# Optimization experiments

Measured on AMD Instinct MI355X. Metric: run time of the kernel, lower is better.

Reference implementation:

```python
import jax, jax.numpy as jnp
import numpy as np

B, CIN, H, W = 32, 16, 64, 64
COUT, K, STRIDE = 32, 3, 1


def setup_inputs() -> dict:
    key = jax.random.key(0)
    k1, k2, k3 = jax.random.split(key, 3)
    x = jax.random.normal(k1, (B, CIN, H, W), dtype=jnp.float32)
    # per-location kernels (Ho, Wo, Cout, Cin, K, K); kaiming-ish scale
    fan_in = CIN * K * K
    bound = float(np.sqrt(3.0 / fan_in))
    weights = jax.random.uniform(k2, (H, W, COUT, CIN, K, K), dtype=jnp.float32,
                                 minval=-bound, maxval=bound)
    bias = jax.random.normal(k3, (H, W, COUT), dtype=jnp.float32)
    return {"x": x, "weights": weights, "bias": bias}


def reference(x, weights, bias):
    Ho, Wo, co, ci, k, _ = weights.shape
    pad = k // 2
    if k % 2 == 1:
        padding = [(pad, pad), (pad, pad)]
    else:
        padding = [(pad - 1, pad), (pad - 1, pad)]
    # im2col: (B, ci*k*k, Ho, Wo); feature dim ordered channel-slowest, matching
    # torch's (C, k, k) flatten after unfold+permute.
    patches = jax.lax.conv_general_dilated_patches(
        x, (k, k), (STRIDE, STRIDE), padding)
    w = weights.reshape(Ho, Wo, co, ci * k * k)
    # per-location matmul: out[b,o,h,w] = sum_p patches[b,p,h,w] * w[h,w,o,p]
    out = jnp.einsum('bphw,hwop->bohw', patches, w)
    out = out + bias.transpose(2, 0, 1)[None]  # (1, Cout, Ho, Wo)
    return out
```

## Files before the change

### kernel.cpp

```cpp
#include <hip/hip_runtime.h>


#define CIN     16
#define HH      64
#define WW      64
#define COUT    32
#define PP      144
#define WT      8
#define RSTRIDE 770

typedef float v4f  __attribute__((ext_vector_type(4)));
typedef float v16f __attribute__((ext_vector_type(16)));
typedef short v8s  __attribute__((ext_vector_type(8)));

__device__ __forceinline__ unsigned short f2bf(float f) {
    unsigned int u = __builtin_bit_cast(unsigned int, f);
    u += 0x7fffu + ((u >> 16) & 1u);
    return (unsigned short)(u >> 16);
}
__device__ __forceinline__ unsigned int pk2(float a, float b) {
    return (unsigned int)f2bf(a) | ((unsigned int)f2bf(b) << 16);
}

__global__ __launch_bounds__(512, 4) void xonv_kernel(
    const float* __restrict__ x,
    const float* __restrict__ weights,
    const float* __restrict__ bias,
    float* __restrict__ out)
{
    const int t  = threadIdx.x;
    const int bi = blockIdx.x;

    const int xcd  = bi & 7;
    const int rest = bi >> 3;
    const int wg   = rest & 7;
    const int h    = (rest >> 3) * 8 + xcd;
    const int w0   = wg * WT;
    const int wstart = w0 - 4;

    __shared__ alignas(16) unsigned char smraw[49280];
    unsigned short* xl = (unsigned short*)smraw;
    float*          ol = (float*)smraw;

    {
        const int rid0 = t >> 2;
        const int sub  = t & 3;
        int b  = rid0 / 48;
        int cr = rid0 % 48;
        const int col4  = wstart + sub * 4;
        const bool colok = (col4 >= 0) && (col4 <= WW - 4);
#pragma unroll
        for (int pass = 0; pass < 12; ++pass) {
            const int c   = cr / 3;
            const int r   = cr - c * 3;
            const int row = h + r - 1;
            float4 f = {0.f, 0.f, 0.f, 0.f};
            if (colok && (unsigned)row < HH) {
                f = *(const float4*)(x + ((size_t)(b * CIN + c)) * (HH * WW)
                                       + row * WW + col4);
            }
            unsigned int* d = (unsigned int*)(xl + b * RSTRIDE + cr * 16 + sub * 4);
            d[0] = pk2(f.x, f.y);
            d[1] = pk2(f.z, f.w);
            b += 2; cr += 32; if (cr >= 48) { cr -= 48; ++b; }
        }
    }
    __syncthreads();

    const int l  = t & 63;
    const int wv = t >> 6;
    const int w  = w0 + wv;
    const int o  = l & 31;
    const int kh = l >> 5;
    const int ph = kh * 8;

    const float* wp = weights + (size_t)(h * WW + w) * (COUT * PP)
                              + (size_t)o * PP + ph;
    const int xbase = (l & 31) * RSTRIDE + wv + 3;

    v16f acc;
#pragma unroll
    for (int i = 0; i < 16; ++i) acc[i] = 0.f;

    int dq = ph >> 2;
    int mq = ph >> 2;

    v4f c0 = *(const v4f*)(wp);
    v4f c1 = *(const v4f*)(wp + 4);

#pragma unroll
    for (int kc = 0; kc < 9; ++kc) {
        v4f n0, n1;
        if (kc < 8) {
            n0 = *(const v4f*)(wp + (kc + 1) * 16);
            n1 = *(const v4f*)(wp + (kc + 1) * 16 + 4);
        }

        v8s a;
        const int base = xbase + dq * 16 + mq;
#pragma unroll
        for (int j = 0; j < 8; ++j) {
            const int e  = mq + j;
            const int tt = (e * 11) >> 5;
            a[j] = (short)xl[base + j + 13 * tt];
        }

        union { unsigned int u[4]; v8s s; } ub;
        ub.u[0] = pk2(c0.x, c0.y); ub.u[1] = pk2(c0.z, c0.w);
        ub.u[2] = pk2(c1.x, c1.y); ub.u[3] = pk2(c1.z, c1.w);

        acc = __builtin_amdgcn_mfma_f32_32x32x16_bf16(a, ub.s, acc, 0, 0, 0);

        c0 = n0; c1 = n1;
        mq += 1; dq += 5; if (mq == 3) { mq = 0; dq += 1; }
    }

    const float bia = bias[(size_t)(h * WW + w) * COUT + o];

    __syncthreads();

#pragma unroll
    for (int r = 0; r < 16; ++r) {
        const int brow = (r & 3) + 8 * (r >> 2) + 4 * kh;
        ol[(brow * COUT + o) * 9 + wv] = acc[r] + bia;
    }
    __syncthreads();

    {
        const int seg = t >> 3;
        const int wj  = t & 7;
        float* ob = out + (size_t)h * WW + w0 + wj;
#pragma unroll
        for (int i = 0; i < 16; ++i) {
            const int bo = i * 64 + seg;
            ob[(size_t)bo * (HH * WW)] = ol[bo * 9 + wj];
        }
    }
}

extern "C" void kernel_launch(void* const* d_in, const int* in_sizes, int n_in,
                              void* d_out, int out_size, void* d_ws, size_t ws_size,
                              hipStream_t stream) {
    const float* x       = (const float*)d_in[0];
    const float* weights = (const float*)d_in[1];
    const float* bias    = (const float*)d_in[2];
    float* out           = (float*)d_out;
    (void)in_sizes; (void)n_in; (void)out_size; (void)d_ws; (void)ws_size;

    dim3 grid(512);
    dim3 block(512);
    hipLaunchKernelGGL(xonv_kernel, grid, block, 0, stream, x, weights, bias, out);
}
```

Baseline: 129.2 us.

## Widen blocks to 16 output columns with compile-time im2col offsets and float4 stores

Each block now covers 16 output columns per row with 1024 threads, which halves the grid and lowers the redundant halo loads of x per output. The shared-memory im2col layout is rebuilt so that gather offsets are compile-time constants, replacing the runtime index arithmetic. Weight prefetch goes two steps ahead, and the first weight loads are issued before the x staging so they overlap it. The epilogue is split into two halves that write float4 vectors to global memory, at the cost of extra barriers and a larger block that may reduce occupancy.

```diff
diff --git a/kernel.cpp b/kernel.cpp
--- a/kernel.cpp
+++ b/kernel.cpp
@@ -1,13 +1,11 @@
 #include <hip/hip_runtime.h>
 
 
-#define CIN     16
-#define HH      64
-#define WW      64
-#define COUT    32
-#define PP      144
-#define WT      8
-#define RSTRIDE 770
+#define CIN  16
+#define HW_  4096
+#define PP   144
+#define RST  20
+#define BST  962
 
 typedef float v4f  __attribute__((ext_vector_type(4)));
 typedef float v16f __attribute__((ext_vector_type(16)));
@@ -21,120 +19,128 @@
 __device__ __forceinline__ unsigned int pk2(float a, float b) {
     return (unsigned int)f2bf(a) | ((unsigned int)f2bf(b) << 16);
 }
+__device__ __forceinline__ constexpr int offp(int p) {
+    const int c = p / 9, rem = p % 9, r = rem / 3, kw = rem % 3;
+    return (c * 3 + r) * RST + kw + 1;
+}
 
-__global__ __launch_bounds__(512, 4) void xonv_kernel(
+__global__ __launch_bounds__(1024, 4) void xonv_kernel(
     const float* __restrict__ x,
-    const float* __restrict__ weights,
+    const float* __restrict__ wt,
     const float* __restrict__ bias,
     float* __restrict__ out)
 {
     const int t  = threadIdx.x;
     const int bi = blockIdx.x;
+    const int h  = ((bi >> 5) << 3) + (bi & 7);
+    const int wg = (bi >> 3) & 3;
+    const int w0 = wg << 4;
 
-    const int xcd  = bi & 7;
-    const int rest = bi >> 3;
-    const int wg   = rest & 7;
-    const int h    = (rest >> 3) * 8 + xcd;
-    const int w0   = wg * WT;
-    const int wstart = w0 - 4;
-
-    __shared__ alignas(16) unsigned char smraw[49280];
-    unsigned short* xl = (unsigned short*)smraw;
-    float*          ol = (float*)smraw;
-
-    {
-        const int rid0 = t >> 2;
-        const int sub  = t & 3;
-        int b  = rid0 / 48;
-        int cr = rid0 % 48;
-        const int col4  = wstart + sub * 4;
-        const bool colok = (col4 >= 0) && (col4 <= WW - 4);
-#pragma unroll
-        for (int pass = 0; pass < 12; ++pass) {
-            const int c   = cr / 3;
-            const int r   = cr - c * 3;
-            const int row = h + r - 1;
-            float4 f = {0.f, 0.f, 0.f, 0.f};
-            if (colok && (unsigned)row < HH) {
-                f = *(const float4*)(x + ((size_t)(b * CIN + c)) * (HH * WW)
-                                       + row * WW + col4);
-            }
-            unsigned int* d = (unsigned int*)(xl + b * RSTRIDE + cr * 16 + sub * 4);
-            d[0] = pk2(f.x, f.y);
-            d[1] = pk2(f.z, f.w);
-            b += 2; cr += 32; if (cr >= 48) { cr -= 48; ++b; }
-        }
-    }
-    __syncthreads();
+    __shared__ unsigned short xs[32 * BST];
+    float* ol = (float*)xs;
 
     const int l  = t & 63;
     const int wv = t >> 6;
     const int w  = w0 + wv;
     const int o  = l & 31;
     const int kh = l >> 5;
-    const int ph = kh * 8;
 
-    const float* wp = weights + (size_t)(h * WW + w) * (COUT * PP)
-                              + (size_t)o * PP + ph;
-    const int xbase = (l & 31) * RSTRIDE + wv + 3;
+    const float* wp = wt + (size_t)(h * 64 + w) * (32 * PP)
+                         + (size_t)o * PP + kh * 8;
+    v4f c00 = *(const v4f*)(wp);
+    v4f c01 = *(const v4f*)(wp + 4);
+    v4f c10 = *(const v4f*)(wp + 16);
+    v4f c11 = *(const v4f*)(wp + 20);
+    const float bia = bias[(size_t)(h * 64 + w) * 32 + o];
+
+    const int wstart = w0 - 4;
+#pragma unroll
+    for (int i = 0; i < 9; ++i) {
+        const int j   = t + i * 1024;
+        const int rid = (int)(((unsigned)j * 43691u) >> 18);
+        const int sub = j - rid * 6;
+        const int b   = (rid * 683) >> 15;
+        const int cr  = rid - b * 48;
+        const int c   = (cr * 43) >> 7;
+        const int r   = cr - c * 3;
+        const int row = h + r - 1;
+        const int col4 = wstart + sub * 4;
+        float4 f = {0.f, 0.f, 0.f, 0.f};
+        if ((unsigned)row < 64u && (unsigned)col4 <= 60u)
+            f = *(const float4*)(x + ((size_t)(b * CIN + c)) * HW_
+                                   + row * 64 + col4);
+        unsigned short* dst = xs + b * BST + cr * RST;
+        if (sub == 0) {
+            ((unsigned int*)dst)[0] = pk2(f.z, f.w);
+        } else if (sub == 5) {
+            ((unsigned int*)dst)[9] = pk2(f.x, f.y);
+        } else {
+            unsigned int* d = (unsigned int*)(dst + sub * 4 - 2);
+            d[0] = pk2(f.x, f.y);
+            d[1] = pk2(f.z, f.w);
+        }
+    }
+    __syncthreads();
+
+    const int gb = o * BST + wv;
 
     v16f acc;
 #pragma unroll
     for (int i = 0; i < 16; ++i) acc[i] = 0.f;
 
-    int dq = ph >> 2;
-    int mq = ph >> 2;
-
-    v4f c0 = *(const v4f*)(wp);
-    v4f c1 = *(const v4f*)(wp + 4);
-
 #pragma unroll
     for (int kc = 0; kc < 9; ++kc) {
         v4f n0, n1;
-        if (kc < 8) {
-            n0 = *(const v4f*)(wp + (kc + 1) * 16);
-            n1 = *(const v4f*)(wp + (kc + 1) * 16 + 4);
+        if (kc < 7) {
+            n0 = *(const v4f*)(wp + (kc + 2) * 16);
+            n1 = *(const v4f*)(wp + (kc + 2) * 16 + 4);
+        } else {
+            n0 = c10; n1 = c11;
         }
 
         v8s a;
-        const int base = xbase + dq * 16 + mq;
 #pragma unroll
         for (int j = 0; j < 8; ++j) {
-            const int e  = mq + j;
-            const int tt = (e * 11) >> 5;
-            a[j] = (short)xl[base + j + 13 * tt];
+            const int C0 = offp(kc * 16 + j);
+            const int C1 = offp(kc * 16 + 8 + j);
+            a[j] = (short)xs[gb + (kh ? C1 : C0)];
         }
 
         union { unsigned int u[4]; v8s s; } ub;
-        ub.u[0] = pk2(c0.x, c0.y); ub.u[1] = pk2(c0.z, c0.w);
-        ub.u[2] = pk2(c1.x, c1.y); ub.u[3] = pk2(c1.z, c1.w);
+        ub.u[0] = pk2(c00.x, c00.y); ub.u[1] = pk2(c00.z, c00.w);
+        ub.u[2] = pk2(c01.x, c01.y); ub.u[3] = pk2(c01.z, c01.w);
 
         acc = __builtin_amdgcn_mfma_f32_32x32x16_bf16(a, ub.s, acc, 0, 0, 0);
 
-        c0 = n0; c1 = n1;
-        mq += 1; dq += 5; if (mq == 3) { mq = 0; dq += 1; }
+        c00 = c10; c01 = c11; c10 = n0; c11 = n1;
     }
-
-    const float bia = bias[(size_t)(h * WW + w) * COUT + o];
 
     __syncthreads();
 
 #pragma unroll
-    for (int r = 0; r < 16; ++r) {
-        const int brow = (r & 3) + 8 * (r >> 2) + 4 * kh;
-        ol[(brow * COUT + o) * 9 + wv] = acc[r] + bia;
-    }
-    __syncthreads();
-
-    {
-        const int seg = t >> 3;
-        const int wj  = t & 7;
-        float* ob = out + (size_t)h * WW + w0 + wj;
+    for (int half = 0; half < 2; ++half) {
 #pragma unroll
-        for (int i = 0; i < 16; ++i) {
-            const int bo = i * 64 + seg;
-            ob[(size_t)bo * (HH * WW)] = ol[bo * 9 + wj];
+        for (int rr = 0; rr < 8; ++rr) {
+            const int r     = half * 8 + rr;
+            const int browl = (r & 3) + 8 * ((r >> 2) & 1) + 4 * kh;
+            ol[(browl * 32 + o) * 17 + wv] = acc[r] + bia;
         }
+        __syncthreads();
+#pragma unroll
+        for (int i2 = 0; i2 < 2; ++i2) {
+            const int flat = t + i2 * 1024;
+            const int bol  = flat >> 2;
+            const int q4   = flat & 3;
+            const int base = bol * 17 + q4 * 4;
+            float4 v;
+            v.x = ol[base + 0]; v.y = ol[base + 1];
+            v.z = ol[base + 2]; v.w = ol[base + 3];
+            const int bg = half * 16 + (bol >> 5);
+            const int og = bol & 31;
+            *(float4*)(out + ((size_t)(bg * 32 + og)) * HW_
+                           + h * 64 + w0 + q4 * 4) = v;
+        }
+        __syncthreads();
     }
 }
 
@@ -147,7 +153,7 @@
     float* out           = (float*)d_out;
     (void)in_sizes; (void)n_in; (void)out_size; (void)d_ws; (void)ws_size;
 
-    dim3 grid(512);
-    dim3 block(512);
+    dim3 grid(256);
+    dim3 block(1024);
     hipLaunchKernelGGL(xonv_kernel, grid, block, 0, stream, x, weights, bias, out);
 }
```

Measured after the change: 125.9 us. -2.6%, faster.

## Stage weights through LDS with coalesced loads and vectorize output stores

Applied to the files above, without the earlier changes.

Weight loads now use contiguous float4 reads per output channel. They are converted to bf16 into a double-buffered per-wave LDS area and read back as B fragments, instead of each lane doing strided 32-byte reads. The x tile layout is changed to compile-time patch offsets with a new row/batch stride, the block-to-(h,w) mapping is reordered, and output stores become float4 writes. The changes add LDS traffic and in-loop LDS writes in exchange for better global coalescing.

```diff
diff --git a/kernel.cpp b/kernel.cpp
--- a/kernel.cpp
+++ b/kernel.cpp
@@ -1,13 +1,10 @@
 #include <hip/hip_runtime.h>
 
 
-#define CIN     16
-#define HH      64
-#define WW      64
-#define COUT    32
-#define PP      144
-#define WT      8
-#define RSTRIDE 770
+#define HW_ 4096
+#define PP  144
+#define RST 14
+#define BST 674
 
 typedef float v4f  __attribute__((ext_vector_type(4)));
 typedef float v16f __attribute__((ext_vector_type(16)));
@@ -21,120 +18,134 @@
 __device__ __forceinline__ unsigned int pk2(float a, float b) {
     return (unsigned int)f2bf(a) | ((unsigned int)f2bf(b) << 16);
 }
+__device__ __forceinline__ constexpr int offp(int p) {
+    const int c = p / 9, rem = p % 9, r = rem / 3, kw = rem % 3;
+    return (c * 3 + r) * RST + kw + 3;
+}
 
 __global__ __launch_bounds__(512, 4) void xonv_kernel(
     const float* __restrict__ x,
-    const float* __restrict__ weights,
+    const float* __restrict__ wt,
     const float* __restrict__ bias,
     float* __restrict__ out)
 {
     const int t  = threadIdx.x;
     const int bi = blockIdx.x;
+    const int xcd  = bi & 7;
+    const int rem  = bi >> 3;
+    const int hsub = rem & 7;
+    const int wg   = rem >> 3;
+    const int h    = xcd * 8 + hsub;
+    const int w0   = wg * 8;
 
-    const int xcd  = bi & 7;
-    const int rest = bi >> 3;
-    const int wg   = rest & 7;
-    const int h    = (rest >> 3) * 8 + xcd;
-    const int w0   = wg * WT;
-    const int wstart = w0 - 4;
+    __shared__ alignas(16) unsigned short xs[21568];
+    __shared__ alignas(16) unsigned short wb[8192];
+    float* ol = (float*)xs;
 
-    __shared__ alignas(16) unsigned char smraw[49280];
-    unsigned short* xl = (unsigned short*)smraw;
-    float*          ol = (float*)smraw;
+    const int l  = t & 63;
+    const int wv = t >> 6;
+    const int o  = l & 31;
+    const int kh = l >> 5;
+    const int w  = w0 + wv;
+
+    const int o2  = (l >> 2) & 15;
+    const int seg = l & 3;
+    const float* wbase = wt + (size_t)((h * 64 + w) * 32) * PP;
+    const float* wp0 = wbase + (size_t)o2 * PP + seg * 4;
+    const float* wp1 = wbase + (size_t)(o2 + 16) * PP + seg * 4;
+
+    float4 c0a = *(const float4*)(wp0);
+    float4 c0b = *(const float4*)(wp1);
+    float4 cua = *(const float4*)(wp0 + 16);
+    float4 cub = *(const float4*)(wp1 + 16);
+
+    const float bia = bias[(size_t)(h * 64 + w) * 32 + o];
 
     {
+        const int sub  = t & 3;
+        const int col4 = w0 - 4 + sub * 4;
+        const bool colok = (col4 >= 0) && (col4 <= 60);
         const int rid0 = t >> 2;
-        const int sub  = t & 3;
-        int b  = rid0 / 48;
-        int cr = rid0 % 48;
-        const int col4  = wstart + sub * 4;
-        const bool colok = (col4 >= 0) && (col4 <= WW - 4);
+        int b  = (rid0 * 683) >> 15;
+        int cr = rid0 - b * 48;
 #pragma unroll
-        for (int pass = 0; pass < 12; ++pass) {
-            const int c   = cr / 3;
+        for (int i = 0; i < 12; ++i) {
+            const int c   = (cr * 43) >> 7;
             const int r   = cr - c * 3;
             const int row = h + r - 1;
             float4 f = {0.f, 0.f, 0.f, 0.f};
-            if (colok && (unsigned)row < HH) {
-                f = *(const float4*)(x + ((size_t)(b * CIN + c)) * (HH * WW)
-                                       + row * WW + col4);
-            }
-            unsigned int* d = (unsigned int*)(xl + b * RSTRIDE + cr * 16 + sub * 4);
+            if (colok && (unsigned)row < 64u)
+                f = *(const float4*)(x + ((size_t)(b * 16 + c)) * HW_
+                                       + row * 64 + col4);
+            unsigned int* d = (unsigned int*)(xs + b * BST + cr * RST + sub * 4);
             d[0] = pk2(f.x, f.y);
             d[1] = pk2(f.z, f.w);
             b += 2; cr += 32; if (cr >= 48) { cr -= 48; ++b; }
         }
     }
+
+    const int wW = wv * 1024;
+    {
+        unsigned int* d0 = (unsigned int*)(wb + wW + o2 * 16 + seg * 4);
+        d0[0] = pk2(c0a.x, c0a.y); d0[1] = pk2(c0a.z, c0a.w);
+        unsigned int* d1 = (unsigned int*)(wb + wW + (o2 + 16) * 16 + seg * 4);
+        d1[0] = pk2(c0b.x, c0b.y); d1[1] = pk2(c0b.z, c0b.w);
+    }
     __syncthreads();
 
-    const int l  = t & 63;
-    const int wv = t >> 6;
-    const int w  = w0 + wv;
-    const int o  = l & 31;
-    const int kh = l >> 5;
-    const int ph = kh * 8;
-
-    const float* wp = weights + (size_t)(h * WW + w) * (COUT * PP)
-                              + (size_t)o * PP + ph;
-    const int xbase = (l & 31) * RSTRIDE + wv + 3;
+    const int gb  = o * BST + wv;
+    const int bfr = wW + o * 16 + kh * 8;
 
     v16f acc;
 #pragma unroll
     for (int i = 0; i < 16; ++i) acc[i] = 0.f;
 
-    int dq = ph >> 2;
-    int mq = ph >> 2;
-
-    v4f c0 = *(const v4f*)(wp);
-    v4f c1 = *(const v4f*)(wp + 4);
-
 #pragma unroll
     for (int kc = 0; kc < 9; ++kc) {
-        v4f n0, n1;
-        if (kc < 8) {
-            n0 = *(const v4f*)(wp + (kc + 1) * 16);
-            n1 = *(const v4f*)(wp + (kc + 1) * 16 + 4);
+        v8s bf = *(const v8s*)(wb + (kc & 1) * 512 + bfr);
+
+        v8s a;
+#pragma unroll
+        for (int j = 0; j < 8; ++j) {
+            const int C0 = offp(kc * 16 + j);
+            const int C1 = offp(kc * 16 + 8 + j);
+            a[j] = (short)xs[gb + (kh ? C1 : C0)];
         }
 
-        v8s a;
-        const int base = xbase + dq * 16 + mq;
-#pragma unroll
-        for (int j = 0; j < 8; ++j) {
-            const int e  = mq + j;
-            const int tt = (e * 11) >> 5;
-            a[j] = (short)xl[base + j + 13 * tt];
+        if (kc < 8) {
+            const int nb = wW + ((kc + 1) & 1) * 512;
+            unsigned int* d0 = (unsigned int*)(wb + nb + o2 * 16 + seg * 4);
+            d0[0] = pk2(cua.x, cua.y); d0[1] = pk2(cua.z, cua.w);
+            unsigned int* d1 = (unsigned int*)(wb + nb + (o2 + 16) * 16 + seg * 4);
+            d1[0] = pk2(cub.x, cub.y); d1[1] = pk2(cub.z, cub.w);
+            if (kc < 7) {
+                cua = *(const float4*)(wp0 + (kc + 2) * 16);
+                cub = *(const float4*)(wp1 + (kc + 2) * 16);
+            }
         }
 
-        union { unsigned int u[4]; v8s s; } ub;
-        ub.u[0] = pk2(c0.x, c0.y); ub.u[1] = pk2(c0.z, c0.w);
-        ub.u[2] = pk2(c1.x, c1.y); ub.u[3] = pk2(c1.z, c1.w);
-
-        acc = __builtin_amdgcn_mfma_f32_32x32x16_bf16(a, ub.s, acc, 0, 0, 0);
-
-        c0 = n0; c1 = n1;
-        mq += 1; dq += 5; if (mq == 3) { mq = 0; dq += 1; }
+        acc = __builtin_amdgcn_mfma_f32_32x32x16_bf16(a, bf, acc, 0, 0, 0);
     }
-
-    const float bia = bias[(size_t)(h * WW + w) * COUT + o];
 
     __syncthreads();
 
 #pragma unroll
     for (int r = 0; r < 16; ++r) {
         const int brow = (r & 3) + 8 * (r >> 2) + 4 * kh;
-        ol[(brow * COUT + o) * 9 + wv] = acc[r] + bia;
+        ol[(brow * 32 + o) * 9 + wv] = acc[r] + bia;
     }
     __syncthreads();
 
-    {
-        const int seg = t >> 3;
-        const int wj  = t & 7;
-        float* ob = out + (size_t)h * WW + w0 + wj;
 #pragma unroll
-        for (int i = 0; i < 16; ++i) {
-            const int bo = i * 64 + seg;
-            ob[(size_t)bo * (HH * WW)] = ol[bo * 9 + wj];
-        }
+    for (int i2 = 0; i2 < 4; ++i2) {
+        const int flat = t + i2 * 512;
+        const int bo   = flat >> 1;
+        const int q4   = flat & 1;
+        const int base = bo * 9 + q4 * 4;
+        float4 v;
+        v.x = ol[base + 0]; v.y = ol[base + 1];
+        v.z = ol[base + 2]; v.w = ol[base + 3];
+        *(float4*)(out + (size_t)bo * HW_ + h * 64 + w0 + q4 * 4) = v;
     }
 }
 
```

Result: no change. 127.6 us (-1.3%).
